# Kernel optimization log

Measured on AMD Instinct MI355X. Metric: run time of the kernel, lower is better.

The kernel has to match this reference:

```python
import jax, jax.numpy as jnp
import numpy as np

N_NODES = 100000
N_EDGES = 1_600_000
F_IN = 500   # PubMed num_node_features
HID = 128
N_CLASSES = 3


def _glorot(key, shape):
    fan_in, fan_out = shape
    limit = np.sqrt(6.0 / (fan_in + fan_out)).astype(np.float32)
    return jax.random.uniform(key, shape, jnp.float32, -limit, limit)


def setup_inputs() -> dict:
    key = jax.random.key(0)
    ks = jax.random.split(key, 8)
    x = jax.random.normal(ks[0], (N_NODES, F_IN), jnp.float32)
    edge_index = jax.random.randint(ks[1], (2, N_EDGES), 0, N_NODES, jnp.int64)
    dims = [(F_IN, HID), (HID, HID), (HID, HID), (HID, HID), (HID, N_CLASSES)]
    inp = {"x": x, "edge_index": edge_index}
    for i, d in enumerate(dims):
        inp[f"W{i+1}"] = _glorot(ks[2 + i], d)
        inp[f"b{i+1}"] = jnp.zeros((d[1],), jnp.float32)
    return inp


def _gcn_conv(h, W, b, src, dst, norm, n):
    # linear transform then normalized neighbor aggregation (scatter-add)
    h = h @ W                                   # [N, out]
    msg = h[src] * norm                         # gather along edges, [E+N, out]
    return jax.ops.segment_sum(msg, dst, num_segments=n) + b


def reference(x, edge_index, W1, b1, W2, b2, W3, b3, W4, b4, W5, b5):
    n = x.shape[0]
    loops = jnp.arange(n)
    src = jnp.concatenate([edge_index[0], loops])  # add self-loops (PyG default)
    dst = jnp.concatenate([edge_index[1], loops])
    # symmetric normalization: deg^{-1/2}[dst] * deg^{-1/2}[src], deg over self-looped graph
    deg = jax.ops.segment_sum(jnp.ones_like(dst, x.dtype), dst, num_segments=n)
    dis = jnp.where(deg > 0, jax.lax.rsqrt(jnp.maximum(deg, 1e-12)), 0.0)
    norm = (dis[src] * dis[dst])[:, None]

    h = jax.nn.relu(_gcn_conv(x, W1, b1, src, dst, norm, n))
    # dropout p=0.5 is identity in eval mode
    h = jax.nn.relu(_gcn_conv(h, W2, b2, src, dst, norm, n))
    h = jax.nn.relu(_gcn_conv(h, W3, b3, src, dst, norm, n))
    h = jax.nn.relu(_gcn_conv(h, W4, b4, src, dst, norm, n))
    return _gcn_conv(h, W5, b5, src, dst, norm, n)
```

## Files before the change

### kernel.cpp

```cpp
#include <hip/hip_runtime.h>
#include <hip/hip_bf16.h>

#define NN 100000
#define NNP 100096
#define NE 1600000
#define FIN 500
#define HID 128
#define LDK 136

typedef __attribute__((ext_vector_type(8))) short short8;
typedef __attribute__((ext_vector_type(4))) float f32x4;

__device__ __forceinline__ float bf2f(unsigned short u) {
    return __uint_as_float(((unsigned int)u) << 16);
}
__device__ __forceinline__ unsigned short f2bf(float f) {
    __hip_bfloat16 h = __float2bfloat16(f);
    return *(unsigned short*)&h;
}
__device__ __forceinline__ float lo16(unsigned int v) { return __uint_as_float(v << 16); }
__device__ __forceinline__ float hi16(unsigned int v) { return __uint_as_float(v & 0xffff0000u); }


__global__ __launch_bounds__(256) void GCNLarge_20761871909627_kernel(int* __restrict__ buf, int n) {
    int i = blockIdx.x * 256 + threadIdx.x;
    if (i < n) buf[i] = 0;
}


__global__ void detect_kernel(const int* __restrict__ ei, const unsigned int* __restrict__ xw,
                              int* __restrict__ flags) {
    int lane = threadIdx.x & 63;
    int any = 0;
    for (int k = lane; k < 128; k += 64) any |= ei[2 * k + 1];
    int hits = 0;
    for (int k = lane; k < 256; k += 64) {
        unsigned e = (xw[k] >> 7) & 0xFF;
        hits += (e >= 100 && e <= 140) ? 1 : 0;
    }
#pragma unroll
    for (int o = 32; o > 0; o >>= 1) {
        any |= __shfl_down(any, o);
        hits += __shfl_down(hits, o);
    }
    if (lane == 0) {
        flags[0] = (any == 0) ? 1 : 0;
        flags[1] = (hits >= 128) ? 1 : 0;
    }
}

__device__ __forceinline__ int edge_src(const int* ei, int e, int m) {
    return m ? ei[2 * (size_t)e] : ei[e];
}
__device__ __forceinline__ int edge_dst(const int* ei, int e, int m) {
    return m ? ei[2 * (size_t)NE + 2 * (size_t)e] : ei[(size_t)NE + e];
}


__global__ __launch_bounds__(256) void count_kernel(const int* __restrict__ ei,
                                                    const int* __restrict__ flags,
                                                    int* __restrict__ cnt) {
    int e = blockIdx.x * 256 + threadIdx.x;
    if (e < NE) {
        int d = edge_dst(ei, e, flags[0]);
        if ((unsigned)d < NN) atomicAdd(&cnt[d], 1);
    }
}

__global__ __launch_bounds__(256) void dis_kernel(const int* __restrict__ cnt,
                                                  float* __restrict__ dis) {
    int i = blockIdx.x * 256 + threadIdx.x;
    if (i < NNP) {
        int c = (i < NN) ? cnt[i] : 0;
        if (c < 0) c = 0;
        dis[i] = rsqrtf((float)(c + 1));
    }
}

__global__ __launch_bounds__(1024) void scan1_kernel(const int* __restrict__ cnt,
                                                     int* __restrict__ off,
                                                     int* __restrict__ bsum) {
    __shared__ int s[1024];
    int i = blockIdx.x * 1024 + threadIdx.x;
    int v = (i < NN) ? cnt[i] : 0;
    s[threadIdx.x] = v;
    __syncthreads();
    for (int d = 1; d < 1024; d <<= 1) {
        int tv = (threadIdx.x >= d) ? s[threadIdx.x - d] : 0;
        __syncthreads();
        s[threadIdx.x] += tv;
        __syncthreads();
    }
    if (i < NN) off[i] = s[threadIdx.x] - v;
    if (threadIdx.x == 1023) bsum[blockIdx.x] = s[1023];
}

__global__ void scan2_kernel(int* __restrict__ bsum, int nb) {
    if (threadIdx.x == 0 && blockIdx.x == 0) {
        int acc = 0;
        for (int b = 0; b < nb; b++) { int v = bsum[b]; bsum[b] = acc; acc += v; }
    }
}

__global__ __launch_bounds__(1024) void scan3_kernel(int* __restrict__ off,
                                                     const int* __restrict__ bsum,
                                                     int* __restrict__ cursor) {
    int i = blockIdx.x * 1024 + threadIdx.x;
    if (i < NN) { int o = off[i] + bsum[blockIdx.x]; off[i] = o; cursor[i] = o; }
    if (i == 0) off[NN] = NE;
}

__global__ __launch_bounds__(256) void place_kernel(const int* __restrict__ ei,
                                                    const int* __restrict__ flags,
                                                    int* __restrict__ cursor,
                                                    int* __restrict__ csr) {
    int e = blockIdx.x * 256 + threadIdx.x;
    if (e < NE) {
        int m = flags[0];
        int s = edge_src(ei, e, m);
        int d = edge_dst(ei, e, m);
        if ((unsigned)s < NN && (unsigned)d < NN) {
            int slot = atomicAdd(&cursor[d], 1);
            if ((unsigned)slot < NE) csr[slot] = s;
        }
    }
}


__global__ __launch_bounds__(256) void wt_kernel(const void* __restrict__ W,
                                                 const int* __restrict__ flags,
                                                 unsigned short* __restrict__ Wt,
                                                 int K, int Kpad, int total) {
    int idx = blockIdx.x * 256 + threadIdx.x;
    if (idx >= total) return;
    int n = idx / Kpad, k = idx - n * Kpad;
    unsigned short v = 0;
    if (k < K) {
        if (flags[1]) v = ((const unsigned short*)W)[(size_t)k * HID + n];
        else          v = f2bf(((const float*)W)[(size_t)k * HID + n]);
    }
    Wt[idx] = v;
}


__global__ __launch_bounds__(256) void gemm128m_kernel(const unsigned short* __restrict__ A,
                                                       const unsigned short* __restrict__ Wt,
                                                       const float* __restrict__ dis,
                                                       unsigned short* __restrict__ out) {
    __shared__ unsigned short As[64 * LDK];
    __shared__ unsigned short Bs[128 * LDK];
    int tid = threadIdx.x;
    int r0 = blockIdx.x * 64;
    for (int idx = tid; idx < 1024; idx += 256) {
        int r = idx >> 4, q = idx & 15;
        *(short8*)&As[r * LDK + q * 8] = *(const short8*)(A + (size_t)(r0 + r) * HID + q * 8);
    }
    for (int idx = tid; idx < 2048; idx += 256) {
        int n = idx >> 4, q = idx & 15;
        *(short8*)&Bs[n * LDK + q * 8] = *(const short8*)(Wt + (size_t)n * HID + q * 8);
    }
    __syncthreads();
    int w = tid >> 6, lane = tid & 63;
    int m = lane & 15, quad = lane >> 4;
    int mbase = (w >> 1) * 32, nbase = (w & 1) * 64;
    f32x4 acc[2][4] = {};
#pragma unroll
    for (int kq = 0; kq < 4; kq++) {
        short8 a0 = *(const short8*)&As[(mbase + m) * LDK + kq * 32 + quad * 8];
        short8 a1 = *(const short8*)&As[(mbase + 16 + m) * LDK + kq * 32 + quad * 8];
#pragma unroll
        for (int nt = 0; nt < 4; nt++) {
            short8 b = *(const short8*)&Bs[(nbase + nt * 16 + m) * LDK + kq * 32 + quad * 8];
            acc[0][nt] = __builtin_amdgcn_mfma_f32_16x16x32_bf16(a0, b, acc[0][nt], 0, 0, 0);
            acc[1][nt] = __builtin_amdgcn_mfma_f32_16x16x32_bf16(a1, b, acc[1][nt], 0, 0, 0);
        }
    }
#pragma unroll
    for (int mt = 0; mt < 2; mt++) {
        int rb = r0 + mbase + mt * 16 + quad * 4;
#pragma unroll
        for (int reg = 0; reg < 4; reg++) {
            float d = dis[rb + reg];
#pragma unroll
            for (int nt = 0; nt < 4; nt++)
                out[(size_t)(rb + reg) * HID + nbase + nt * 16 + m] = f2bf(acc[mt][nt][reg] * d);
        }
    }
}


__global__ __launch_bounds__(256) void gemm1m_kernel(const void* __restrict__ Av,
                                                     const unsigned short* __restrict__ Wt1,
                                                     const float* __restrict__ dis,
                                                     const int* __restrict__ flags,
                                                     unsigned short* __restrict__ out) {
    __shared__ unsigned short As[64 * LDK];
    __shared__ unsigned short Bs[128 * LDK];
    int tid = threadIdx.x;
    int r0 = blockIdx.x * 64;
    int bf = flags[1];
    int w = tid >> 6, lane = tid & 63;
    int m = lane & 15, quad = lane >> 4;
    int mbase = (w >> 1) * 32, nbase = (w & 1) * 64;
    f32x4 acc[2][4] = {};
    for (int kc = 0; kc < 4; kc++) {
        int k0 = kc * 128;
        __syncthreads();
        for (int idx = tid; idx < 2048; idx += 256) {
            int r = idx >> 5, q = idx & 31;
            int grow = r0 + r; if (grow >= NN) grow = NN - 1;
            int kk = k0 + q * 4;
            ushort4 val;
            if (kk + 4 <= FIN) {
                if (bf) val = *(const ushort4*)((const unsigned short*)Av + (size_t)grow * FIN + kk);
                else {
                    const float* fp = (const float*)Av + (size_t)grow * FIN + kk;
                    val = make_ushort4(f2bf(fp[0]), f2bf(fp[1]), f2bf(fp[2]), f2bf(fp[3]));
                }
            } else val = make_ushort4(0, 0, 0, 0);
            *(ushort4*)&As[r * LDK + q * 4] = val;
        }
        for (int idx = tid; idx < 2048; idx += 256) {
            int n = idx >> 4, q = idx & 15;
            *(short8*)&Bs[n * LDK + q * 8] = *(const short8*)(Wt1 + (size_t)n * 512 + k0 + q * 8);
        }
        __syncthreads();
#pragma unroll
        for (int kq = 0; kq < 4; kq++) {
            short8 a0 = *(const short8*)&As[(mbase + m) * LDK + kq * 32 + quad * 8];
            short8 a1 = *(const short8*)&As[(mbase + 16 + m) * LDK + kq * 32 + quad * 8];
#pragma unroll
            for (int nt = 0; nt < 4; nt++) {
                short8 b = *(const short8*)&Bs[(nbase + nt * 16 + m) * LDK + kq * 32 + quad * 8];
                acc[0][nt] = __builtin_amdgcn_mfma_f32_16x16x32_bf16(a0, b, acc[0][nt], 0, 0, 0);
                acc[1][nt] = __builtin_amdgcn_mfma_f32_16x16x32_bf16(a1, b, acc[1][nt], 0, 0, 0);
            }
        }
    }
#pragma unroll
    for (int mt = 0; mt < 2; mt++) {
        int rb = r0 + mbase + mt * 16 + quad * 4;
#pragma unroll
        for (int reg = 0; reg < 4; reg++) {
            int row = rb + reg;
            if (row < NN) {
                float d = dis[row];
#pragma unroll
                for (int nt = 0; nt < 4; nt++)
                    out[(size_t)row * HID + nbase + nt * 16 + m] = f2bf(acc[mt][nt][reg] * d);
            }
        }
    }
}


__global__ __launch_bounds__(256) void aggb_kernel(const unsigned short* __restrict__ tin,
                                                   const int* __restrict__ off,
                                                   const int* __restrict__ csr,
                                                   const float* __restrict__ dis,
                                                   const void* __restrict__ bias,
                                                   const int* __restrict__ flags,
                                                   unsigned short* __restrict__ hout,
                                                   int relu, int scale_src) {
    int node = blockIdx.x * 4 + (threadIdx.x >> 6);
    int lane = threadIdx.x & 63;
    float di = dis[node];
    unsigned int sv = *(const unsigned int*)(tin + (size_t)node * HID + lane * 2);
    float acc0 = scale_src ? di * lo16(sv) : lo16(sv);
    float acc1 = scale_src ? di * hi16(sv) : hi16(sv);
    int e0 = off[node], e1 = off[node + 1];
    if (e0 < 0) e0 = 0;
    if (e1 > NE) e1 = NE;
    int e = e0;
    if (!scale_src) {
        for (; e + 4 <= e1; e += 4) {
            int i0 = csr[e], i1 = csr[e + 1], i2 = csr[e + 2], i3 = csr[e + 3];
            unsigned int v0 = *(const unsigned int*)(tin + (size_t)i0 * HID + lane * 2);
            unsigned int v1 = *(const unsigned int*)(tin + (size_t)i1 * HID + lane * 2);
            unsigned int v2 = *(const unsigned int*)(tin + (size_t)i2 * HID + lane * 2);
            unsigned int v3 = *(const unsigned int*)(tin + (size_t)i3 * HID + lane * 2);
            acc0 += lo16(v0); acc1 += hi16(v0);
            acc0 += lo16(v1); acc1 += hi16(v1);
            acc0 += lo16(v2); acc1 += hi16(v2);
            acc0 += lo16(v3); acc1 += hi16(v3);
        }
        for (; e < e1; e++) {
            int s = csr[e];
            unsigned int v = *(const unsigned int*)(tin + (size_t)s * HID + lane * 2);
            acc0 += lo16(v); acc1 += hi16(v);
        }
    } else {
        for (; e + 4 <= e1; e += 4) {
            int i0 = csr[e], i1 = csr[e + 1], i2 = csr[e + 2], i3 = csr[e + 3];
            unsigned int v0 = *(const unsigned int*)(tin + (size_t)i0 * HID + lane * 2);
            unsigned int v1 = *(const unsigned int*)(tin + (size_t)i1 * HID + lane * 2);
            unsigned int v2 = *(const unsigned int*)(tin + (size_t)i2 * HID + lane * 2);
            unsigned int v3 = *(const unsigned int*)(tin + (size_t)i3 * HID + lane * 2);
            float m0 = dis[i0], m1 = dis[i1], m2 = dis[i2], m3 = dis[i3];
            acc0 += m0 * lo16(v0); acc1 += m0 * hi16(v0);
            acc0 += m1 * lo16(v1); acc1 += m1 * hi16(v1);
            acc0 += m2 * lo16(v2); acc1 += m2 * hi16(v2);
            acc0 += m3 * lo16(v3); acc1 += m3 * hi16(v3);
        }
        for (; e < e1; e++) {
            int s = csr[e];
            unsigned int v = *(const unsigned int*)(tin + (size_t)s * HID + lane * 2);
            float mm = dis[s];
            acc0 += mm * lo16(v); acc1 += mm * hi16(v);
        }
    }
    float o0 = di * acc0, o1 = di * acc1;
    if (bias) {
        if (flags[1]) { o0 += bf2f(((const unsigned short*)bias)[lane * 2]);
                        o1 += bf2f(((const unsigned short*)bias)[lane * 2 + 1]); }
        else          { o0 += ((const float*)bias)[lane * 2];
                        o1 += ((const float*)bias)[lane * 2 + 1]; }
    }
    if (relu) { o0 = fmaxf(o0, 0.f); o1 = fmaxf(o1, 0.f); }
    unsigned int pk = ((unsigned int)f2bf(o1) << 16) | (unsigned int)f2bf(o0);
    *(unsigned int*)(hout + (size_t)node * HID + lane * 2) = pk;
}


__global__ __launch_bounds__(256) void gemm5_kernel(const unsigned short* __restrict__ A,
                                                    const void* __restrict__ W5v,
                                                    const void* __restrict__ b5v,
                                                    const int* __restrict__ flags,
                                                    void* __restrict__ outv) {
    __shared__ float Ws[384];
    __shared__ float bs[3];
    int tid = threadIdx.x;
    int bf = flags[1];
    for (int idx = tid; idx < 384; idx += 256)
        Ws[idx] = bf ? bf2f(((const unsigned short*)W5v)[idx]) : ((const float*)W5v)[idx];
    if (tid < 3)
        bs[tid] = bf ? bf2f(((const unsigned short*)b5v)[tid]) : ((const float*)b5v)[tid];
    __syncthreads();
    int lane = tid & 63;
    int row = blockIdx.x * 4 + (tid >> 6);
    float a0 = bf2f(A[(size_t)row * HID + lane]);
    float a1 = bf2f(A[(size_t)row * HID + 64 + lane]);
    float c0 = a0 * Ws[lane * 3 + 0] + a1 * Ws[(lane + 64) * 3 + 0];
    float c1 = a0 * Ws[lane * 3 + 1] + a1 * Ws[(lane + 64) * 3 + 1];
    float c2 = a0 * Ws[lane * 3 + 2] + a1 * Ws[(lane + 64) * 3 + 2];
#pragma unroll
    for (int o = 32; o > 0; o >>= 1) {
        c0 += __shfl_down(c0, o);
        c1 += __shfl_down(c1, o);
        c2 += __shfl_down(c2, o);
    }
    if (lane == 0) {
        c0 += bs[0]; c1 += bs[1]; c2 += bs[2];
        if (bf) {
            unsigned short* out = (unsigned short*)outv;
            out[(size_t)row * 3 + 0] = f2bf(c0);
            out[(size_t)row * 3 + 1] = f2bf(c1);
            out[(size_t)row * 3 + 2] = f2bf(c2);
        } else {
            float* out = (float*)outv;
            out[(size_t)row * 3 + 0] = c0;
            out[(size_t)row * 3 + 1] = c1;
            out[(size_t)row * 3 + 2] = c2;
        }
    }
}

extern "C" void kernel_launch(void* const* d_in, const int* in_sizes, int n_in,
                              void* d_out, int out_size, void* d_ws, size_t ws_size,
                              hipStream_t stream) {
    const void* x = nullptr; const int* ei = nullptr;
    const void* W1 = nullptr; const void* W5 = nullptr; const void* b5 = nullptr;
    const void* Wmid[3] = {nullptr, nullptr, nullptr};
    const void* bvec[4] = {nullptr, nullptr, nullptr, nullptr};
    int nw = 0, nb = 0;
    for (int i = 0; i < n_in; i++) {
        int s = in_sizes[i];
        if      (s == 50000000) x = d_in[i];
        else if (s == 3200000)  ei = (const int*)d_in[i];
        else if (s == 64000)    W1 = d_in[i];
        else if (s == 16384)  { if (nw < 3) Wmid[nw++] = d_in[i]; }
        else if (s == 384)      W5 = d_in[i];
        else if (s == 128)    { if (nb < 4) bvec[nb++] = d_in[i]; }
        else if (s == 3)        b5 = d_in[i];
    }
    if (!x || !ei || !W1 || !W5 || !b5 || nw < 3 || nb < 4) return;

    char* p = (char*)d_ws;
    auto alloc = [&](size_t bytes) { char* q = p; p += (bytes + 255) & ~(size_t)255; return (void*)q; };
    int*   flags = (int*)alloc(256);
    float* dis   = (float*)alloc((size_t)NNP * 4);
    int*   cnt   = (int*)alloc((size_t)NN * 4);
    int*   off   = (int*)alloc((size_t)(NN + 1) * 4);
    int*   cur   = (int*)alloc((size_t)NN * 4);
    int*   bsum  = (int*)alloc(128 * 4);
    int*   csr   = (int*)alloc((size_t)NE * 4);
    unsigned short* Wt1 = (unsigned short*)alloc((size_t)128 * 512 * 2);
    unsigned short* Wt2 = (unsigned short*)alloc((size_t)128 * 128 * 2);
    unsigned short* Wt3 = (unsigned short*)alloc((size_t)128 * 128 * 2);
    unsigned short* Wt4 = (unsigned short*)alloc((size_t)128 * 128 * 2);
    unsigned short* T   = (unsigned short*)alloc((size_t)NNP * HID * 2);
    unsigned short* H   = (unsigned short*)alloc((size_t)NNP * HID * 2);

    GCNLarge_20761871909627_kernel<<<(NN + 255) / 256, 256, 0, stream>>>(cnt, NN);
    detect_kernel<<<1, 64, 0, stream>>>(ei, (const unsigned int*)x, flags);
    wt_kernel<<<256, 256, 0, stream>>>(W1, flags, Wt1, FIN, 512, 128 * 512);
    wt_kernel<<<64, 256, 0, stream>>>(Wmid[0], flags, Wt2, HID, 128, 128 * 128);
    wt_kernel<<<64, 256, 0, stream>>>(Wmid[1], flags, Wt3, HID, 128, 128 * 128);
    wt_kernel<<<64, 256, 0, stream>>>(Wmid[2], flags, Wt4, HID, 128, 128 * 128);
    count_kernel<<<(NE + 255) / 256, 256, 0, stream>>>(ei, flags, cnt);
    dis_kernel<<<(NNP + 255) / 256, 256, 0, stream>>>(cnt, dis);
    scan1_kernel<<<98, 1024, 0, stream>>>(cnt, off, bsum);
    scan2_kernel<<<1, 64, 0, stream>>>(bsum, 98);
    scan3_kernel<<<98, 1024, 0, stream>>>(off, bsum, cur);
    place_kernel<<<(NE + 255) / 256, 256, 0, stream>>>(ei, flags, cur, csr);

    const int GB = NNP / 64;
    gemm1m_kernel<<<GB, 256, 0, stream>>>(x, Wt1, dis, flags, T);
    aggb_kernel<<<NN / 4, 256, 0, stream>>>(T, off, csr, dis, bvec[0], flags, H, 1, 0);
    gemm128m_kernel<<<GB, 256, 0, stream>>>(H, Wt2, dis, T);
    aggb_kernel<<<NN / 4, 256, 0, stream>>>(T, off, csr, dis, bvec[1], flags, H, 1, 0);
    gemm128m_kernel<<<GB, 256, 0, stream>>>(H, Wt3, dis, T);
    aggb_kernel<<<NN / 4, 256, 0, stream>>>(T, off, csr, dis, bvec[2], flags, H, 1, 0);
    gemm128m_kernel<<<GB, 256, 0, stream>>>(H, Wt4, dis, T);
    aggb_kernel<<<NN / 4, 256, 0, stream>>>(T, off, csr, dis, bvec[3], flags, H, 1, 0);
    aggb_kernel<<<NN / 4, 256, 0, stream>>>(H, off, csr, dis, nullptr, flags, T, 0, 1);
    gemm5_kernel<<<NN / 4, 256, 0, stream>>>(T, W5, b5, flags, d_out);
}
```

Baseline: 1.014 ms.

## Drop LDS staging in GEMMs, keep weights in registers, unroll aggregation gathers by 8

Both GEMM kernels now load A and B fragments directly from global memory into registers instead of staging through shared memory with barriers. The 128-wide GEMM keeps the weight fragments resident in registers and processes four 64-row tiles per block, double-buffering the next A tile's loads. The aggregation kernel unrolls its neighbor gather loop from 4 to 8 to keep more loads in flight. The cost is more register pressure, which can lower occupancy, and uncoalesced direct global fragment loads in place of cooperative LDS fills.

```diff
diff --git a/kernel.cpp b/kernel.cpp
--- a/kernel.cpp
+++ b/kernel.cpp
@@ -6,7 +6,6 @@
 #define NE 1600000
 #define FIN 500
 #define HID 128
-#define LDK 136
 
 typedef __attribute__((ext_vector_type(8))) short short8;
 typedef __attribute__((ext_vector_type(4))) float f32x4;
@@ -143,99 +142,113 @@
 }
 
 
-__global__ __launch_bounds__(256) void gemm128m_kernel(const unsigned short* __restrict__ A,
-                                                       const unsigned short* __restrict__ Wt,
-                                                       const float* __restrict__ dis,
-                                                       unsigned short* __restrict__ out) {
-    __shared__ unsigned short As[64 * LDK];
-    __shared__ unsigned short Bs[128 * LDK];
+__global__ __launch_bounds__(256) void gemmWr_kernel(const unsigned short* __restrict__ A,
+                                                     const unsigned short* __restrict__ Wt,
+                                                     const float* __restrict__ dis,
+                                                     unsigned short* __restrict__ out) {
     int tid = threadIdx.x;
-    int r0 = blockIdx.x * 64;
-    for (int idx = tid; idx < 1024; idx += 256) {
-        int r = idx >> 4, q = idx & 15;
-        *(short8*)&As[r * LDK + q * 8] = *(const short8*)(A + (size_t)(r0 + r) * HID + q * 8);
-    }
-    for (int idx = tid; idx < 2048; idx += 256) {
-        int n = idx >> 4, q = idx & 15;
-        *(short8*)&Bs[n * LDK + q * 8] = *(const short8*)(Wt + (size_t)n * HID + q * 8);
-    }
-    __syncthreads();
     int w = tid >> 6, lane = tid & 63;
     int m = lane & 15, quad = lane >> 4;
     int mbase = (w >> 1) * 32, nbase = (w & 1) * 64;
-    f32x4 acc[2][4] = {};
-#pragma unroll
-    for (int kq = 0; kq < 4; kq++) {
-        short8 a0 = *(const short8*)&As[(mbase + m) * LDK + kq * 32 + quad * 8];
-        short8 a1 = *(const short8*)&As[(mbase + 16 + m) * LDK + kq * 32 + quad * 8];
-#pragma unroll
-        for (int nt = 0; nt < 4; nt++) {
-            short8 b = *(const short8*)&Bs[(nbase + nt * 16 + m) * LDK + kq * 32 + quad * 8];
-            acc[0][nt] = __builtin_amdgcn_mfma_f32_16x16x32_bf16(a0, b, acc[0][nt], 0, 0, 0);
-            acc[1][nt] = __builtin_amdgcn_mfma_f32_16x16x32_bf16(a1, b, acc[1][nt], 0, 0, 0);
-        }
-    }
-#pragma unroll
-    for (int mt = 0; mt < 2; mt++) {
-        int rb = r0 + mbase + mt * 16 + quad * 4;
-#pragma unroll
-        for (int reg = 0; reg < 4; reg++) {
-            float d = dis[rb + reg];
-#pragma unroll
-            for (int nt = 0; nt < 4; nt++)
-                out[(size_t)(rb + reg) * HID + nbase + nt * 16 + m] = f2bf(acc[mt][nt][reg] * d);
-        }
-    }
-}
-
-
-__global__ __launch_bounds__(256) void gemm1m_kernel(const void* __restrict__ Av,
+    short8 b[4][4];
+#pragma unroll
+    for (int nt = 0; nt < 4; nt++)
+#pragma unroll
+        for (int kq = 0; kq < 4; kq++)
+            b[nt][kq] = *(const short8*)(Wt + (size_t)(nbase + nt * 16 + m) * HID + kq * 32 + quad * 8);
+    int t0 = blockIdx.x * 4;
+    short8 aP[4][2], aQ[4][2];
+    auto loadA = [&](int t, short8 a[4][2]) {
+        const unsigned short* p0 = A + (size_t)(t * 64 + mbase + m) * HID + quad * 8;
+        const unsigned short* p1 = p0 + (size_t)16 * HID;
+#pragma unroll
+        for (int kq = 0; kq < 4; kq++) {
+            a[kq][0] = *(const short8*)(p0 + kq * 32);
+            a[kq][1] = *(const short8*)(p1 + kq * 32);
+        }
+    };
+    loadA(t0, aP);
+#pragma unroll
+    for (int tt = 0; tt < 4; tt++) {
+        if (tt < 3) loadA(t0 + tt + 1, (tt & 1) ? aP : aQ);
+        short8 (*ac)[2] = (tt & 1) ? aQ : aP;
+        f32x4 acc[2][4] = {};
+#pragma unroll
+        for (int kq = 0; kq < 4; kq++)
+#pragma unroll
+            for (int nt = 0; nt < 4; nt++) {
+                acc[0][nt] = __builtin_amdgcn_mfma_f32_16x16x32_bf16(ac[kq][0], b[nt][kq], acc[0][nt], 0, 0, 0);
+                acc[1][nt] = __builtin_amdgcn_mfma_f32_16x16x32_bf16(ac[kq][1], b[nt][kq], acc[1][nt], 0, 0, 0);
+            }
+        int r0 = (t0 + tt) * 64;
+#pragma unroll
+        for (int mt = 0; mt < 2; mt++) {
+            int rb = r0 + mbase + mt * 16 + quad * 4;
+#pragma unroll
+            for (int reg = 0; reg < 4; reg++) {
+                float d = dis[rb + reg];
+#pragma unroll
+                for (int nt = 0; nt < 4; nt++)
+                    out[(size_t)(rb + reg) * HID + nbase + nt * 16 + m] = f2bf(acc[mt][nt][reg] * d);
+            }
+        }
+    }
+}
+
+
+__global__ __launch_bounds__(256) void gemm1r_kernel(const void* __restrict__ Av,
                                                      const unsigned short* __restrict__ Wt1,
                                                      const float* __restrict__ dis,
                                                      const int* __restrict__ flags,
                                                      unsigned short* __restrict__ out) {
-    __shared__ unsigned short As[64 * LDK];
-    __shared__ unsigned short Bs[128 * LDK];
     int tid = threadIdx.x;
-    int r0 = blockIdx.x * 64;
     int bf = flags[1];
     int w = tid >> 6, lane = tid & 63;
     int m = lane & 15, quad = lane >> 4;
     int mbase = (w >> 1) * 32, nbase = (w & 1) * 64;
+    int r0 = blockIdx.x * 64;
+    int row0 = r0 + mbase + m;       int rc0 = (row0 < NN) ? row0 : NN - 1;
+    int row1 = r0 + mbase + 16 + m;  int rc1 = (row1 < NN) ? row1 : NN - 1;
     f32x4 acc[2][4] = {};
+#pragma unroll
     for (int kc = 0; kc < 4; kc++) {
-        int k0 = kc * 128;
-        __syncthreads();
-        for (int idx = tid; idx < 2048; idx += 256) {
-            int r = idx >> 5, q = idx & 31;
-            int grow = r0 + r; if (grow >= NN) grow = NN - 1;
-            int kk = k0 + q * 4;
-            ushort4 val;
-            if (kk + 4 <= FIN) {
-                if (bf) val = *(const ushort4*)((const unsigned short*)Av + (size_t)grow * FIN + kk);
-                else {
-                    const float* fp = (const float*)Av + (size_t)grow * FIN + kk;
-                    val = make_ushort4(f2bf(fp[0]), f2bf(fp[1]), f2bf(fp[2]), f2bf(fp[3]));
+        short8 b[4][4];
+#pragma unroll
+        for (int nt = 0; nt < 4; nt++)
+#pragma unroll
+            for (int kq = 0; kq < 4; kq++)
+                b[nt][kq] = *(const short8*)(Wt1 + (size_t)(nbase + nt * 16 + m) * 512 + kc * 128 + kq * 32 + quad * 8);
+        short8 a[4][2];
+#pragma unroll
+        for (int kq = 0; kq < 4; kq++) {
+            int k_off = kc * 128 + kq * 32 + quad * 8;
+            ushort4 z = make_ushort4(0, 0, 0, 0);
+#pragma unroll
+            for (int mt = 0; mt < 2; mt++) {
+                int rr = mt ? rc1 : rc0;
+                ushort4 lo = z, hi = z;
+                if (bf) {
+                    const unsigned short* xp = (const unsigned short*)Av + (size_t)rr * FIN + k_off;
+                    if (k_off + 4 <= FIN) lo = *(const ushort4*)xp;
+                    if (k_off + 8 <= FIN) hi = *(const ushort4*)(xp + 4);
+                } else {
+                    const float* xp = (const float*)Av + (size_t)rr * FIN + k_off;
+                    if (k_off + 4 <= FIN) { float4 f = *(const float4*)xp;
+                        lo = make_ushort4(f2bf(f.x), f2bf(f.y), f2bf(f.z), f2bf(f.w)); }
+                    if (k_off + 8 <= FIN) { float4 f = *(const float4*)(xp + 4);
+                        hi = make_ushort4(f2bf(f.x), f2bf(f.y), f2bf(f.z), f2bf(f.w)); }
                 }
-            } else val = make_ushort4(0, 0, 0, 0);
-            *(ushort4*)&As[r * LDK + q * 4] = val;
-        }
-        for (int idx = tid; idx < 2048; idx += 256) {
-            int n = idx >> 4, q = idx & 15;
-            *(short8*)&Bs[n * LDK + q * 8] = *(const short8*)(Wt1 + (size_t)n * 512 + k0 + q * 8);
-        }
-        __syncthreads();
-#pragma unroll
-        for (int kq = 0; kq < 4; kq++) {
-            short8 a0 = *(const short8*)&As[(mbase + m) * LDK + kq * 32 + quad * 8];
-            short8 a1 = *(const short8*)&As[(mbase + 16 + m) * LDK + kq * 32 + quad * 8];
+                a[kq][mt] = short8{(short)lo.x, (short)lo.y, (short)lo.z, (short)lo.w,
+                                   (short)hi.x, (short)hi.y, (short)hi.z, (short)hi.w};
+            }
+        }
+#pragma unroll
+        for (int kq = 0; kq < 4; kq++)
 #pragma unroll
             for (int nt = 0; nt < 4; nt++) {
-                short8 b = *(const short8*)&Bs[(nbase + nt * 16 + m) * LDK + kq * 32 + quad * 8];
-                acc[0][nt] = __builtin_amdgcn_mfma_f32_16x16x32_bf16(a0, b, acc[0][nt], 0, 0, 0);
-                acc[1][nt] = __builtin_amdgcn_mfma_f32_16x16x32_bf16(a1, b, acc[1][nt], 0, 0, 0);
+                acc[0][nt] = __builtin_amdgcn_mfma_f32_16x16x32_bf16(a[kq][0], b[nt][kq], acc[0][nt], 0, 0, 0);
+                acc[1][nt] = __builtin_amdgcn_mfma_f32_16x16x32_bf16(a[kq][1], b[nt][kq], acc[1][nt], 0, 0, 0);
             }
-        }
     }
 #pragma unroll
     for (int mt = 0; mt < 2; mt++) {
@@ -273,16 +286,30 @@
     if (e1 > NE) e1 = NE;
     int e = e0;
     if (!scale_src) {
+        for (; e + 8 <= e1; e += 8) {
+            int i0 = csr[e],     i1 = csr[e + 1], i2 = csr[e + 2], i3 = csr[e + 3];
+            int i4 = csr[e + 4], i5 = csr[e + 5], i6 = csr[e + 6], i7 = csr[e + 7];
+            unsigned int v0 = *(const unsigned int*)(tin + (size_t)i0 * HID + lane * 2);
+            unsigned int v1 = *(const unsigned int*)(tin + (size_t)i1 * HID + lane * 2);
+            unsigned int v2 = *(const unsigned int*)(tin + (size_t)i2 * HID + lane * 2);
+            unsigned int v3 = *(const unsigned int*)(tin + (size_t)i3 * HID + lane * 2);
+            unsigned int v4 = *(const unsigned int*)(tin + (size_t)i4 * HID + lane * 2);
+            unsigned int v5 = *(const unsigned int*)(tin + (size_t)i5 * HID + lane * 2);
+            unsigned int v6 = *(const unsigned int*)(tin + (size_t)i6 * HID + lane * 2);
+            unsigned int v7 = *(const unsigned int*)(tin + (size_t)i7 * HID + lane * 2);
+            acc0 += lo16(v0); acc1 += hi16(v0); acc0 += lo16(v1); acc1 += hi16(v1);
+            acc0 += lo16(v2); acc1 += hi16(v2); acc0 += lo16(v3); acc1 += hi16(v3);
+            acc0 += lo16(v4); acc1 += hi16(v4); acc0 += lo16(v5); acc1 += hi16(v5);
+            acc0 += lo16(v6); acc1 += hi16(v6); acc0 += lo16(v7); acc1 += hi16(v7);
+        }
         for (; e + 4 <= e1; e += 4) {
             int i0 = csr[e], i1 = csr[e + 1], i2 = csr[e + 2], i3 = csr[e + 3];
             unsigned int v0 = *(const unsigned int*)(tin + (size_t)i0 * HID + lane * 2);
             unsigned int v1 = *(const unsigned int*)(tin + (size_t)i1 * HID + lane * 2);
             unsigned int v2 = *(const unsigned int*)(tin + (size_t)i2 * HID + lane * 2);
             unsigned int v3 = *(const unsigned int*)(tin + (size_t)i3 * HID + lane * 2);
-            acc0 += lo16(v0); acc1 += hi16(v0);
-            acc0 += lo16(v1); acc1 += hi16(v1);
-            acc0 += lo16(v2); acc1 += hi16(v2);
-            acc0 += lo16(v3); acc1 += hi16(v3);
+            acc0 += lo16(v0); acc1 += hi16(v0); acc0 += lo16(v1); acc1 += hi16(v1);
+            acc0 += lo16(v2); acc1 += hi16(v2); acc0 += lo16(v3); acc1 += hi16(v3);
         }
         for (; e < e1; e++) {
             int s = csr[e];
@@ -290,17 +317,27 @@
             acc0 += lo16(v); acc1 += hi16(v);
         }
     } else {
-        for (; e + 4 <= e1; e += 4) {
-            int i0 = csr[e], i1 = csr[e + 1], i2 = csr[e + 2], i3 = csr[e + 3];
+        for (; e + 8 <= e1; e += 8) {
+            int i0 = csr[e],     i1 = csr[e + 1], i2 = csr[e + 2], i3 = csr[e + 3];
+            int i4 = csr[e + 4], i5 = csr[e + 5], i6 = csr[e + 6], i7 = csr[e + 7];
             unsigned int v0 = *(const unsigned int*)(tin + (size_t)i0 * HID + lane * 2);
             unsigned int v1 = *(const unsigned int*)(tin + (size_t)i1 * HID + lane * 2);
             unsigned int v2 = *(const unsigned int*)(tin + (size_t)i2 * HID + lane * 2);
             unsigned int v3 = *(const unsigned int*)(tin + (size_t)i3 * HID + lane * 2);
+            unsigned int v4 = *(const unsigned int*)(tin + (size_t)i4 * HID + lane * 2);
+            unsigned int v5 = *(const unsigned int*)(tin + (size_t)i5 * HID + lane * 2);
+            unsigned int v6 = *(const unsigned int*)(tin + (size_t)i6 * HID + lane * 2);
+            unsigned int v7 = *(const unsigned int*)(tin + (size_t)i7 * HID + lane * 2);
             float m0 = dis[i0], m1 = dis[i1], m2 = dis[i2], m3 = dis[i3];
+            float m4 = dis[i4], m5 = dis[i5], m6 = dis[i6], m7 = dis[i7];
             acc0 += m0 * lo16(v0); acc1 += m0 * hi16(v0);
             acc0 += m1 * lo16(v1); acc1 += m1 * hi16(v1);
             acc0 += m2 * lo16(v2); acc1 += m2 * hi16(v2);
             acc0 += m3 * lo16(v3); acc1 += m3 * hi16(v3);
+            acc0 += m4 * lo16(v4); acc1 += m4 * hi16(v4);
+            acc0 += m5 * lo16(v5); acc1 += m5 * hi16(v5);
+            acc0 += m6 * lo16(v6); acc1 += m6 * hi16(v6);
+            acc0 += m7 * lo16(v7); acc1 += m7 * hi16(v7);
         }
         for (; e < e1; e++) {
             int s = csr[e];
@@ -414,14 +451,13 @@
     scan3_kernel<<<98, 1024, 0, stream>>>(off, bsum, cur);
     place_kernel<<<(NE + 255) / 256, 256, 0, stream>>>(ei, flags, cur, csr);
 
-    const int GB = NNP / 64;
-    gemm1m_kernel<<<GB, 256, 0, stream>>>(x, Wt1, dis, flags, T);
+    gemm1r_kernel<<<NNP / 64, 256, 0, stream>>>(x, Wt1, dis, flags, T);
     aggb_kernel<<<NN / 4, 256, 0, stream>>>(T, off, csr, dis, bvec[0], flags, H, 1, 0);
-    gemm128m_kernel<<<GB, 256, 0, stream>>>(H, Wt2, dis, T);
+    gemmWr_kernel<<<NNP / 256, 256, 0, stream>>>(H, Wt2, dis, T);
     aggb_kernel<<<NN / 4, 256, 0, stream>>>(T, off, csr, dis, bvec[1], flags, H, 1, 0);
-    gemm128m_kernel<<<GB, 256, 0, stream>>>(H, Wt3, dis, T);
+    gemmWr_kernel<<<NNP / 256, 256, 0, stream>>>(H, Wt3, dis, T);
     aggb_kernel<<<NN / 4, 256, 0, stream>>>(T, off, csr, dis, bvec[2], flags, H, 1, 0);
-    gemm128m_kernel<<<GB, 256, 0, stream>>>(H, Wt4, dis, T);
+    gemmWr_kernel<<<NNP / 256, 256, 0, stream>>>(H, Wt4, dis, T);
     aggb_kernel<<<NN / 4, 256, 0, stream>>>(T, off, csr, dis, bvec[3], flags, H, 1, 0);
     aggb_kernel<<<NN / 4, 256, 0, stream>>>(H, off, csr, dis, nullptr, flags, T, 0, 1);
     gemm5_kernel<<<NN / 4, 256, 0, stream>>>(T, W5, b5, flags, d_out);
```

Result: no change. 1.003 ms (-1.0%).
